# Optimization experiments

Hardware: AMD Instinct MI355X
Metric: run time of the kernel (lower is better)

## Reference

```python
import jax, jax.numpy as jnp
import numpy as np

B, IDF, CDF, SIZE, H, L = 32, 64, 256, 32, 8, 256
SS = SIZE * SIZE  # size*size = 1024


def setup_inputs() -> dict:
    key = jax.random.key(0)
    k1, k2, k3 = jax.random.split(key, 3)
    return {
        "weightedContext": jax.random.normal(k1, (B, IDF, SS), dtype=jnp.float32),
        "context": jax.random.normal(k2, (B, CDF, L), dtype=jnp.float32),
        # per-head conv1x1 weights: [H, size*size, cdf]
        "W": jax.random.normal(k3, (H, SS, CDF), dtype=jnp.float32) * 0.02,
        "ih": SIZE,
        "iw": SIZE,
    }


def reference(weightedContext, context, W, ih, iw):
    batch, idf = weightedContext.shape[0], weightedContext.shape[1]
    # conv1x1 per head == per-head GEMM over channel dim: [B,H,SS,L]
    sourceC = jnp.einsum("hoc,bcl->bhol", W, context)
    # attention scores: [B,H,idf,L]
    attn = jnp.einsum("bio,bhol->bhil", weightedContext, sourceC)
    # softmax over sourceL (nn.Softmax() on 2D view -> dim=1 == L here)
    attn = jax.nn.softmax(attn, axis=-1)
    # weightedContext_T summed over heads: bmm(sourceC, attn^T) -> [B,idf,SS]
    ctx_out = jnp.einsum("bhol,bhil->bio", sourceC, attn)
    ctx_out = ctx_out.reshape(batch, idf, ih, iw)
    # attnOut: per-head attn transposed [B,L,idf], summed over heads
    attn_out = jnp.sum(attn, axis=1).transpose(0, 2, 1)
    return ctx_out, attn_out
```

## Files before the change

kernel.cpp:

```cpp
#include <hip/hip_runtime.h>
#include <hip/hip_bf16.h>

#define BB 32
#define IDF 64
#define CDF 256
#define SSZ 1024
#define NH 8
#define LL 256
#define KHC 2048

typedef __attribute__((ext_vector_type(8))) _Float16 half8v;
typedef __attribute__((ext_vector_type(4))) float f32x4;

#define GLDS16(g, l) __builtin_amdgcn_global_load_lds(                        \
    (const __attribute__((address_space(1))) void*)(g),                       \
    (__attribute__((address_space(3))) void*)(l), 16, 0, 0)

#define WAIT_ENTER3(NFULL, NHALF)                                             \
  { if (ks < NSTEP - 2)                                                       \
      asm volatile("s_waitcnt vmcnt(" #NFULL ")" ::: "memory");               \
    else if (ks == NSTEP - 2)                                                 \
      asm volatile("s_waitcnt vmcnt(" #NHALF ")" ::: "memory");               \
    else                                                                      \
      asm volatile("s_waitcnt vmcnt(0)" ::: "memory");                        \
    __builtin_amdgcn_s_barrier();                                             \
    __builtin_amdgcn_sched_barrier(0); }
#define BAR_EXIT()                                                            \
  { __builtin_amdgcn_sched_barrier(0);                                        \
    __builtin_amdgcn_s_barrier();                                             \
    __builtin_amdgcn_sched_barrier(0); }
#define LDS_BAR()                                                             \
  { asm volatile("s_waitcnt lgkmcnt(0)" ::: "memory");                        \
    __builtin_amdgcn_s_barrier();                                             \
    __builtin_amdgcn_sched_barrier(0); }

__device__ inline unsigned short f2h(float x) {
  _Float16 h = (_Float16)x;
  return *reinterpret_cast<unsigned short*>(&h);
}
__device__ inline float h2f(unsigned short u) {
  _Float16 h = *reinterpret_cast<_Float16*>(&u);
  return (float)h;
}

__global__ __launch_bounds__(256) void k_prep(const float* __restrict__ wc,
                                              const float* __restrict__ W,
                                              const float* __restrict__ ctx,
                                              unsigned short* __restrict__ wc16,
                                              unsigned short* __restrict__ W16,
                                              unsigned short* __restrict__ ctx16,
                                              unsigned short* __restrict__ Wt16,
                                              unsigned short* __restrict__ cT16) {
  __shared__ float Tt[64][65];
  int blk0 = blockIdx.x;
  int t = threadIdx.x;
  if (blk0 < 6144) {
    int sel = blk0 >> 11;
    int idx = ((blk0 & 2047) * 256 + t) * 4;
    const float* src = (sel == 0) ? wc : (sel == 1) ? W : ctx;
    unsigned short* d = (sel == 0) ? wc16 : (sel == 1) ? W16 : ctx16;
    float4 v = *reinterpret_cast<const float4*>(&src[idx]);
    __align__(8) unsigned short h[4] = {f2h(v.x), f2h(v.y), f2h(v.z), f2h(v.w)};
    *reinterpret_cast<int2*>(&d[idx]) = *reinterpret_cast<int2*>(h);
  } else if (blk0 < 6656) {
    int blk = blk0 - 6144;
    int h = blk >> 6, ot = (blk >> 2) & 15, cq = blk & 3;
    int og = ot * 64, cg = cq * 64;
    int o_l = t >> 4, c4 = (t & 15) * 4;
#pragma unroll
    for (int p = 0; p < 4; ++p) {
      int o = o_l + 16 * p;
      float4 v = *reinterpret_cast<const float4*>(
          &W[((size_t)h * SSZ + og + o) * CDF + cg + c4]);
      Tt[c4 + 0][o] = v.x; Tt[c4 + 1][o] = v.y;
      Tt[c4 + 2][o] = v.z; Tt[c4 + 3][o] = v.w;
    }
    __syncthreads();
    int c_l = t >> 2;
#pragma unroll
    for (int p = 0; p < 4; ++p) {
      int o0 = ((t & 3) + 4 * p) * 4;
      __align__(8) unsigned short hv[4];
#pragma unroll
      for (int j = 0; j < 4; ++j) hv[j] = f2h(Tt[c_l][o0 + j]);
      size_t base = ((size_t)h * CDF + cg + c_l) * SSZ + og + o0;
      *reinterpret_cast<int2*>(&Wt16[base]) = *reinterpret_cast<int2*>(hv);
    }
  } else {
    int blk = blk0 - 6656;
    int b = blk >> 4, cq = (blk >> 2) & 3, lt = blk & 3;
    int cg = cq * 64, lg = lt * 64;
    int c_l = t >> 4, l4 = (t & 15) * 4;
#pragma unroll
    for (int p = 0; p < 4; ++p) {
      int c = c_l + 16 * p;
      float4 v = *reinterpret_cast<const float4*>(
          &ctx[((size_t)b * CDF + cg + c) * LL + lg + l4]);
      Tt[l4 + 0][c] = v.x; Tt[l4 + 1][c] = v.y;
      Tt[l4 + 2][c] = v.z; Tt[l4 + 3][c] = v.w;
    }
    __syncthreads();
    int l_l = t >> 2;
#pragma unroll
    for (int p = 0; p < 4; ++p) {
      int c0 = ((t & 3) + 4 * p) * 4;
      __align__(8) unsigned short hv[4];
#pragma unroll
      for (int j = 0; j < 4; ++j) hv[j] = f2h(Tt[l_l][c0 + j]);
      size_t base = ((size_t)b * LL + lg + l_l) * CDF + cg + c0;
      *reinterpret_cast<int2*>(&cT16[base]) = *reinterpret_cast<int2*>(hv);
    }
  }
}

__device__ __forceinline__ void st_p1(short* dst, const short* gA, const short* gB,
                                      int wave, int lane, int k0) {
#pragma unroll
  for (int j = 0; j < 3; ++j) {
    int inst = wave * 3 + j;
    const short* src; int toff, rb;
    if (inst < 4)       { src = gA; toff = 0;     rb = inst * 16; }
    else if (inst < 20) { src = gB; toff = 2048;  rb = (inst - 4) * 16; }
    else                { src = gA; toff = 10240; rb = (inst - 20) * 16; }
    int r  = rb + (lane >> 2);
    int gc = (lane & 3) ^ ((r >> 1) & 3);
    GLDS16(src + (size_t)r * SSZ + k0 + gc * 8, dst + toff + rb * 32);
  }
}
__device__ __forceinline__ void st_pB(short* dst, const short* gB, int ld,
                                      int wave, int lane, int k0) {
#pragma unroll
  for (int j = 0; j < 2; ++j) {
    int inst = wave * 2 + j;
    int rb = inst * 16;
    int r  = rb + (lane >> 2);
    int gc = (lane & 3) ^ ((r >> 1) & 3);
    GLDS16(gB + (size_t)r * ld + k0 + gc * 8, dst + 2048 + rb * 32);
  }
}

__global__ __launch_bounds__(512) void k123(const unsigned short* __restrict__ wc16,
                                            const unsigned short* __restrict__ Wt16,
                                            const unsigned short* __restrict__ cT16,
                                            const unsigned short* __restrict__ ctx16,
                                            unsigned short* __restrict__ P16,
                                            unsigned short* __restrict__ N216) {
  __shared__ __align__(16) short S[3 * 12288 + 16384];
  short* M_lds = &S[3 * 12288];

  int bh = blockIdx.x;
  int b = bh >> 3, h = bh & 7;
  int t = threadIdx.x;
  int lane = t & 63, wave = t >> 6;
  int ln15 = lane & 15, kh = lane >> 4;
  int rowq = (lane >> 4) * 4;

  const short* gA = (const short*)wc16 + (size_t)b * IDF * SSZ;
  const short* gB = (const short*)Wt16 + (size_t)h * CDF * SSZ;
  const short* gT = (const short*)cT16 + (size_t)b * LL * CDF;
  const short* gC = (const short*)ctx16 + (size_t)b * CDF * LL;

  int offA[4], offB[2], rowM[4], rmask[4];
#pragma unroll
  for (int r = 0; r < 4; ++r) {
    int row = r * 16 + ln15;
    offA[r] = row * 32 + ((kh ^ ((row >> 1) & 3)) * 8);
    rowM[r] = row * 256;
    rmask[r] = row & 7;
  }
#pragma unroll
  for (int c = 0; c < 2; ++c) {
    int row = wave * 32 + c * 16 + ln15;
    offB[c] = 2048 + row * 32 + ((kh ^ ((row >> 1) & 3)) * 8);
  }

  f32x4 acc[4][2] = {};

  st_p1(&S[0],         gA, gB, wave, lane, 0);
  st_p1(&S[12288],     gA, gB, wave, lane, 32);
  st_p1(&S[2 * 12288], gA, gB, wave, lane, 64);
  int cur = 0;
  {
    const int NSTEP = 32;
#pragma unroll 1
    for (int ks = 0; ks < NSTEP; ++ks) {
      short* Sc = &S[cur * 12288];
      WAIT_ENTER3(6, 3)
      half8v fa[4], fb[2];
#pragma unroll
      for (int r = 0; r < 4; ++r)
        fa[r] = *reinterpret_cast<const half8v*>(&Sc[offA[r]]);
#pragma unroll
      for (int c = 0; c < 2; ++c)
        fb[c] = *reinterpret_cast<const half8v*>(&Sc[offB[c]]);
      __builtin_amdgcn_s_setprio(1);
#pragma unroll
      for (int r = 0; r < 4; ++r)
#pragma unroll
        for (int c = 0; c < 2; ++c)
          acc[r][c] = __builtin_amdgcn_mfma_f32_16x16x32_f16(fa[r], fb[c], acc[r][c], 0, 0, 0);
      __builtin_amdgcn_s_setprio(0);
      BAR_EXIT()
      if (ks + 3 < NSTEP)
        st_p1(Sc, gA, gB, wave, lane, (ks + 3) * 32);
      cur = (cur == 2) ? 0 : cur + 1;
    }
  }
#pragma unroll
  for (int r = 0; r < 4; ++r)
#pragma unroll
    for (int c = 0; c < 2; ++c)
#pragma unroll
      for (int reg = 0; reg < 4; ++reg) {
        int row = r * 16 + rowq + reg;
        int col = wave * 32 + c * 16 + ln15;
        M_lds[row * 256 + ((((col >> 3) ^ (row & 7)) << 3) + (col & 7))] =
            (short)f2h(acc[r][c][reg]);
      }
  LDS_BAR()

#pragma unroll
  for (int r = 0; r < 4; ++r)
#pragma unroll
    for (int c = 0; c < 2; ++c) acc[r][c] = (f32x4){0.f, 0.f, 0.f, 0.f};
  st_pB(&S[0],         gT, CDF, wave, lane, 0);
  st_pB(&S[12288],     gT, CDF, wave, lane, 32);
  st_pB(&S[2 * 12288], gT, CDF, wave, lane, 64);
  cur = 0;
  {
    const int NSTEP = 8;
#pragma unroll 1
    for (int ks = 0; ks < NSTEP; ++ks) {
      short* Sc = &S[cur * 12288];
      WAIT_ENTER3(4, 2)
      half8v fa[4], fb[2];
#pragma unroll
      for (int r = 0; r < 4; ++r) {
        int ck = ((ks * 4 + kh) ^ rmask[r]) << 3;
        fa[r] = *reinterpret_cast<const half8v*>(&M_lds[rowM[r] + ck]);
      }
#pragma unroll
      for (int c = 0; c < 2; ++c)
        fb[c] = *reinterpret_cast<const half8v*>(&Sc[offB[c]]);
      __builtin_amdgcn_s_setprio(1);
#pragma unroll
      for (int r = 0; r < 4; ++r)
#pragma unroll
        for (int c = 0; c < 2; ++c)
          acc[r][c] = __builtin_amdgcn_mfma_f32_16x16x32_f16(fa[r], fb[c], acc[r][c], 0, 0, 0);
      __builtin_amdgcn_s_setprio(0);
      BAR_EXIT()
      if (ks + 3 < NSTEP)
        st_pB(Sc, gT, CDF, wave, lane, (ks + 3) * 32);
      cur = (cur == 2) ? 0 : cur + 1;
    }
  }

  st_pB(&S[0],         gC, LL, wave, lane, 0);
  st_pB(&S[12288],     gC, LL, wave, lane, 32);
  st_pB(&S[2 * 12288], gC, LL, wave, lane, 64);

  float* pm = reinterpret_cast<float*>(M_lds);
  float gmax[4][4], ginv[4][4];
#pragma unroll
  for (int r = 0; r < 4; ++r)
#pragma unroll
    for (int reg = 0; reg < 4; ++reg) {
      float m = fmaxf(acc[r][0][reg], acc[r][1][reg]);
#pragma unroll
      for (int msk = 8; msk >= 1; msk >>= 1) m = fmaxf(m, __shfl_xor(m, msk, 64));
      if (ln15 == 0) pm[(r * 16 + rowq + reg) * 8 + wave] = m;
    }
  LDS_BAR()
#pragma unroll
  for (int r = 0; r < 4; ++r)
#pragma unroll
    for (int reg = 0; reg < 4; ++reg) {
      int row = r * 16 + rowq + reg;
      float4 p0 = *reinterpret_cast<const float4*>(&pm[row * 8]);
      float4 p1 = *reinterpret_cast<const float4*>(&pm[row * 8 + 4]);
      gmax[r][reg] = fmaxf(fmaxf(fmaxf(p0.x, p0.y), fmaxf(p0.z, p0.w)),
                           fmaxf(fmaxf(p1.x, p1.y), fmaxf(p1.z, p1.w)));
    }
  LDS_BAR()
#pragma unroll
  for (int r = 0; r < 4; ++r)
#pragma unroll
    for (int reg = 0; reg < 4; ++reg) {
      acc[r][0][reg] = __expf(acc[r][0][reg] - gmax[r][reg]);
      acc[r][1][reg] = __expf(acc[r][1][reg] - gmax[r][reg]);
      float s = acc[r][0][reg] + acc[r][1][reg];
#pragma unroll
      for (int msk = 8; msk >= 1; msk >>= 1) s += __shfl_xor(s, msk, 64);
      if (ln15 == 0) pm[(r * 16 + rowq + reg) * 8 + wave] = s;
    }
  LDS_BAR()
#pragma unroll
  for (int r = 0; r < 4; ++r)
#pragma unroll
    for (int reg = 0; reg < 4; ++reg) {
      int row = r * 16 + rowq + reg;
      float4 p0 = *reinterpret_cast<const float4*>(&pm[row * 8]);
      float4 p1 = *reinterpret_cast<const float4*>(&pm[row * 8 + 4]);
      ginv[r][reg] = 1.f / (p0.x + p0.y + p0.z + p0.w + p1.x + p1.y + p1.z + p1.w);
    }
  LDS_BAR()

  size_t pbase = (size_t)bh * IDF * LL;
#pragma unroll
  for (int r = 0; r < 4; ++r)
#pragma unroll
    for (int c = 0; c < 2; ++c)
#pragma unroll
      for (int reg = 0; reg < 4; ++reg) {
        float p = acc[r][c][reg] * ginv[r][reg];
        int row = r * 16 + rowq + reg;
        int col = wave * 32 + c * 16 + ln15;
        unsigned short ph = f2h(p);
        P16[pbase + (size_t)row * LL + col] = ph;
        M_lds[row * 256 + ((((col >> 3) ^ (row & 7)) << 3) + (col & 7))] = (short)ph;
      }
  LDS_BAR()

#pragma unroll
  for (int r = 0; r < 4; ++r)
#pragma unroll
    for (int c = 0; c < 2; ++c) acc[r][c] = (f32x4){0.f, 0.f, 0.f, 0.f};
  cur = 0;
  {
    const int NSTEP = 8;
#pragma unroll 1
    for (int ks = 0; ks < NSTEP; ++ks) {
      short* Sc = &S[cur * 12288];
      WAIT_ENTER3(4, 2)
      half8v fa[4], fb[2];
#pragma unroll
      for (int r = 0; r < 4; ++r) {
        int ck = ((ks * 4 + kh) ^ rmask[r]) << 3;
        fa[r] = *reinterpret_cast<const half8v*>(&M_lds[rowM[r] + ck]);
      }
#pragma unroll
      for (int c = 0; c < 2; ++c)
        fb[c] = *reinterpret_cast<const half8v*>(&Sc[offB[c]]);
      __builtin_amdgcn_s_setprio(1);
#pragma unroll
      for (int r = 0; r < 4; ++r)
#pragma unroll
        for (int c = 0; c < 2; ++c)
          acc[r][c] = __builtin_amdgcn_mfma_f32_16x16x32_f16(fa[r], fb[c], acc[r][c], 0, 0, 0);
      __builtin_amdgcn_s_setprio(0);
      BAR_EXIT()
      if (ks + 3 < NSTEP)
        st_pB(Sc, gC, LL, wave, lane, (ks + 3) * 32);
      cur = (cur == 2) ? 0 : cur + 1;
    }
  }

  size_t nbase = (size_t)b * IDF * KHC + h * CDF;
#pragma unroll
  for (int r = 0; r < 4; ++r)
#pragma unroll
    for (int c = 0; c < 2; ++c)
#pragma unroll
      for (int reg = 0; reg < 4; ++reg) {
        size_t idx = nbase + (size_t)(r * 16 + rowq + reg) * KHC + wave * 32 + c * 16 + ln15;
        N216[idx] = f2h(acc[r][c][reg]);
      }
}

__device__ __forceinline__ void k4_stage(short* dst,
                                         const short* gA, const short* gB,
                                         int wave, int lane, int kk0, int obase) {
  int h4 = kk0 >> 8, cb = kk0 & 255;
#pragma unroll
  for (int j = 0; j < 3; ++j) {
    int inst = wave * 3 + j;
    if (inst < 4) {
      int rb = inst * 16;
      int r  = rb + (lane >> 2);
      int gc = (lane & 3) ^ ((r >> 1) & 3);
      GLDS16(gA + (size_t)r * KHC + kk0 + gc * 8, dst + rb * 32);
    } else {
      int rb = (inst - 4) * 16;
      int r  = rb + (lane >> 2);
      int gc = (lane & 3) ^ ((r >> 1) & 3);
      GLDS16(gB + (size_t)(h4 * SSZ + obase + r) * CDF + cb + gc * 8,
             dst + 2048 + rb * 32);
    }
  }
}

__global__ __launch_bounds__(256) void k4_mfma(const unsigned short* __restrict__ N216,
                                               const unsigned short* __restrict__ W16,
                                               float* __restrict__ out0,
                                               float* __restrict__ out1) {
  __shared__ __align__(16) short S[3 * 6144];

  int blk = blockIdx.x;
  int g = blk >> 8;
  int r8 = blk & 255;
  int b = r8 >> 3, ot = r8 & 7;
  int obase = ot * 128;
  int t = threadIdx.x;
  int lane = t & 63, wave = t >> 6;
  int ln15 = lane & 15, kh = lane >> 4;

  const short* gA = (const short*)N216 + (size_t)b * IDF * KHC;
  const short* gB = (const short*)W16;

  int offA[4], offB[2];
#pragma unroll
  for (int r = 0; r < 4; ++r) {
    int row = r * 16 + ln15;
    offA[r] = row * 32 + ((kh ^ ((row >> 1) & 3)) * 8);
  }
#pragma unroll
  for (int c = 0; c < 2; ++c) {
    int row = wave * 32 + c * 16 + ln15;
    offB[c] = 2048 + row * 32 + ((kh ^ ((row >> 1) & 3)) * 8);
  }

  int kbase = g * (KHC / 2);
  f32x4 acc[4][2] = {};

  k4_stage(&S[0],        gA, gB, wave, lane, kbase, obase);
  k4_stage(&S[6144],     gA, gB, wave, lane, kbase + 32, obase);
  k4_stage(&S[2 * 6144], gA, gB, wave, lane, kbase + 64, obase);
  int cur = 0;

  const int NSTEP = 32;
#pragma unroll 1
  for (int ks = 0; ks < NSTEP; ++ks) {
    short* Sc = &S[cur * 6144];
    WAIT_ENTER3(6, 3)
    half8v fa[4], fb[2];
#pragma unroll
    for (int r = 0; r < 4; ++r)
      fa[r] = *reinterpret_cast<const half8v*>(&Sc[offA[r]]);
#pragma unroll
    for (int c = 0; c < 2; ++c)
      fb[c] = *reinterpret_cast<const half8v*>(&Sc[offB[c]]);
    __builtin_amdgcn_s_setprio(1);
#pragma unroll
    for (int r = 0; r < 4; ++r)
#pragma unroll
      for (int c = 0; c < 2; ++c)
        acc[r][c] = __builtin_amdgcn_mfma_f32_16x16x32_f16(fa[r], fb[c], acc[r][c], 0, 0, 0);
    __builtin_amdgcn_s_setprio(0);
    BAR_EXIT()
    if (ks + 3 < NSTEP)
      k4_stage(Sc, gA, gB, wave, lane, kbase + (ks + 3) * 32, obase);
    cur = (cur == 2) ? 0 : cur + 1;
  }

  float* dst = (g == 0) ? out0 : out1;
  int rowq = (lane >> 4) * 4;
#pragma unroll
  for (int r = 0; r < 4; ++r)
#pragma unroll
    for (int c = 0; c < 2; ++c)
#pragma unroll
      for (int reg = 0; reg < 4; ++reg)
        dst[((size_t)b * IDF + r * 16 + rowq + reg) * SSZ +
            obase + wave * 32 + c * 16 + ln15] = acc[r][c][reg];
}

__global__ __launch_bounds__(256) void k_epi(const unsigned short* __restrict__ P16,
                                             float* __restrict__ outa,
                                             float* __restrict__ out,
                                             const float* __restrict__ Pbuf) {
  int blk0 = blockIdx.x;
  int tid = threadIdx.x;
  if (blk0 >= 128) {
    int idx = (blk0 - 128) * 256 + tid;
    float4 a = reinterpret_cast<float4*>(out)[idx];
    float4 p = reinterpret_cast<const float4*>(Pbuf)[idx];
    a.x += p.x; a.y += p.y; a.z += p.z; a.w += p.w;
    reinterpret_cast<float4*>(out)[idx] = a;
    return;
  }
  __shared__ float T[64][65];
  int b = blk0 >> 2, lt = blk0 & 3;
  int l0 = lt * 64;
  float4 acc[4];
#pragma unroll
  for (int p = 0; p < 4; ++p) acc[p] = make_float4(0.f, 0.f, 0.f, 0.f);
  for (int h = 0; h < NH; ++h) {
    size_t src = (size_t)(b * NH + h) * IDF * LL;
#pragma unroll
    for (int p = 0; p < 4; ++p) {
      int f = tid + p * 256;
      int i = f >> 4, lc = (f & 15) * 4;
      ushort4 u = *reinterpret_cast<const ushort4*>(&P16[src + i * LL + l0 + lc]);
      acc[p].x += h2f(u.x); acc[p].y += h2f(u.y);
      acc[p].z += h2f(u.z); acc[p].w += h2f(u.w);
    }
  }
#pragma unroll
  for (int p = 0; p < 4; ++p) {
    int f = tid + p * 256;
    int i = f >> 4, lc = (f & 15) * 4;
    T[i][lc + 0] = acc[p].x; T[i][lc + 1] = acc[p].y;
    T[i][lc + 2] = acc[p].z; T[i][lc + 3] = acc[p].w;
  }
  __syncthreads();
#pragma unroll
  for (int p = 0; p < 4; ++p) {
    int f = tid + p * 256;
    int lr = f >> 4, ic = (f & 15) * 4;
    float4 v = {T[ic + 0][lr], T[ic + 1][lr], T[ic + 2][lr], T[ic + 3][lr]};
    *reinterpret_cast<float4*>(&outa[((size_t)b * LL + l0 + lr) * IDF + ic]) = v;
  }
}

extern "C" void kernel_launch(void* const* d_in, const int* in_sizes, int n_in,
                              void* d_out, int out_size, void* d_ws, size_t ws_size,
                              hipStream_t stream) {
  const float* wc  = (const float*)d_in[0];
  const float* ctx = (const float*)d_in[1];
  const float* W   = (const float*)d_in[2];
  float* out = (float*)d_out;

  const size_t NE = 2097152;
  const size_t NM = 4194304;
  unsigned short* p = (unsigned short*)d_ws;
  unsigned short *wc16 = p;   p += NE;
  unsigned short *Wt16 = p;   p += NE;
  unsigned short *W16  = p;   p += NE;
  unsigned short *ctx16 = p;  p += NE;
  unsigned short *cT16 = p;   p += NE;
  unsigned short *P16  = p;   p += NM;
  unsigned short *N216 = p;   p += NM;
  float* Pbuf = (float*)p;

  k_prep  <<<7168, 256, 0, stream>>>(wc, W, ctx, wc16, W16, ctx16, Wt16, cT16);
  k123    <<<BB * NH, 512, 0, stream>>>(wc16, Wt16, cT16, ctx16, P16, N216);
  k4_mfma <<<512, 256, 0, stream>>>(N216, W16, out, Pbuf);
  k_epi   <<<2176, 256, 0, stream>>>(P16, out + (size_t)BB * IDF * SSZ, out, Pbuf);
}
```

Measured before the change: 79.78 us.

## Split first GEMM into separate kernel with doubled grid for more parallelism

The first GEMM stage (wc × W per head, K=1024) moves out of the fused k123 kernel into a new k1_mfma kernel. It launches 512 blocks of 256 threads, splitting the CDF dimension in half and writing an fp16 intermediate M16 to global memory. The remaining k23 kernel then streams M16 in place of the long K loop. The aim is better occupancy and CU utilisation than the 256 blocks that each ran a 32-step loop. The cost is an extra kernel launch and a global round trip for the 64x256 intermediate per (b,h).

```diff
diff --git a/kernel.cpp b/kernel.cpp
--- a/kernel.cpp
+++ b/kernel.cpp
@@ -113,18 +113,109 @@
   }
 }
 
-__device__ __forceinline__ void st_p1(short* dst, const short* gA, const short* gB,
+__device__ __forceinline__ void k1_stage(short* dst,
+                                         const short* gA, const short* gB,
+                                         int wave, int lane, int k0) {
+#pragma unroll
+  for (int j = 0; j < 3; ++j) {
+    int inst = wave * 3 + j;
+    if (inst < 4) {
+      int rb = inst * 16;
+      int r  = rb + (lane >> 2);
+      int gc = (lane & 3) ^ ((r >> 1) & 3);
+      GLDS16(gA + (size_t)r * SSZ + k0 + gc * 8, dst + rb * 32);
+    } else {
+      int rb = (inst - 4) * 16;
+      int r  = rb + (lane >> 2);
+      int gc = (lane & 3) ^ ((r >> 1) & 3);
+      GLDS16(gB + (size_t)r * SSZ + k0 + gc * 8, dst + 2048 + rb * 32);
+    }
+  }
+}
+
+__global__ __launch_bounds__(256) void k1_mfma(const unsigned short* __restrict__ wc16,
+                                               const unsigned short* __restrict__ Wt16,
+                                               unsigned short* __restrict__ M16) {
+  __shared__ __align__(16) short S[3 * 6144];
+
+  int blk = blockIdx.x;
+  int bh = blk >> 1, nh = blk & 1;
+  int b = bh >> 3, h = bh & 7;
+  int t = threadIdx.x;
+  int lane = t & 63, wave = t >> 6;
+  int ln15 = lane & 15, kh = lane >> 4;
+
+  const short* gA = (const short*)wc16 + (size_t)b * IDF * SSZ;
+  const short* gB = (const short*)Wt16 + (size_t)(h * CDF + nh * 128) * SSZ;
+
+  int offA[4], offB[2];
+#pragma unroll
+  for (int r = 0; r < 4; ++r) {
+    int row = r * 16 + ln15;
+    offA[r] = row * 32 + ((kh ^ ((row >> 1) & 3)) * 8);
+  }
+#pragma unroll
+  for (int c = 0; c < 2; ++c) {
+    int row = wave * 32 + c * 16 + ln15;
+    offB[c] = 2048 + row * 32 + ((kh ^ ((row >> 1) & 3)) * 8);
+  }
+
+  f32x4 acc[4][2] = {};
+  k1_stage(&S[0],        gA, gB, wave, lane, 0);
+  k1_stage(&S[6144],     gA, gB, wave, lane, 32);
+  k1_stage(&S[2 * 6144], gA, gB, wave, lane, 64);
+  int cur = 0;
+
+  const int NSTEP = 32;
+#pragma unroll 1
+  for (int ks = 0; ks < NSTEP; ++ks) {
+    short* Sc = &S[cur * 6144];
+    WAIT_ENTER3(6, 3)
+    half8v fa[4], fb[2];
+#pragma unroll
+    for (int r = 0; r < 4; ++r)
+      fa[r] = *reinterpret_cast<const half8v*>(&Sc[offA[r]]);
+#pragma unroll
+    for (int c = 0; c < 2; ++c)
+      fb[c] = *reinterpret_cast<const half8v*>(&Sc[offB[c]]);
+    __builtin_amdgcn_s_setprio(1);
+#pragma unroll
+    for (int r = 0; r < 4; ++r)
+#pragma unroll
+      for (int c = 0; c < 2; ++c)
+        acc[r][c] = __builtin_amdgcn_mfma_f32_16x16x32_f16(fa[r], fb[c], acc[r][c], 0, 0, 0);
+    __builtin_amdgcn_s_setprio(0);
+    BAR_EXIT()
+    if (ks + 3 < NSTEP)
+      k1_stage(Sc, gA, gB, wave, lane, (ks + 3) * 32);
+    cur = (cur == 2) ? 0 : cur + 1;
+  }
+
+  size_t obase = (size_t)bh * IDF * CDF + nh * 128;
+  int rowq = (lane >> 4) * 4;
+#pragma unroll
+  for (int r = 0; r < 4; ++r)
+#pragma unroll
+    for (int c = 0; c < 2; ++c)
+#pragma unroll
+      for (int reg = 0; reg < 4; ++reg) {
+        size_t idx = obase + (size_t)(r * 16 + rowq + reg) * CDF + wave * 32 + c * 16 + ln15;
+        M16[idx] = f2h(acc[r][c][reg]);
+      }
+}
+
+__device__ __forceinline__ void st_p2(short* dst, const short* gM, const short* gT,
                                       int wave, int lane, int k0) {
 #pragma unroll
   for (int j = 0; j < 3; ++j) {
     int inst = wave * 3 + j;
     const short* src; int toff, rb;
-    if (inst < 4)       { src = gA; toff = 0;     rb = inst * 16; }
-    else if (inst < 20) { src = gB; toff = 2048;  rb = (inst - 4) * 16; }
-    else                { src = gA; toff = 10240; rb = (inst - 20) * 16; }
+    if (inst < 4)       { src = gM; toff = 0;     rb = inst * 16; }
+    else if (inst < 20) { src = gT; toff = 2048;  rb = (inst - 4) * 16; }
+    else                { src = gM; toff = 10240; rb = (inst - 20) * 16; }
     int r  = rb + (lane >> 2);
     int gc = (lane & 3) ^ ((r >> 1) & 3);
-    GLDS16(src + (size_t)r * SSZ + k0 + gc * 8, dst + toff + rb * 32);
+    GLDS16(src + (size_t)r * CDF + k0 + gc * 8, dst + toff + rb * 32);
   }
 }
 __device__ __forceinline__ void st_pB(short* dst, const short* gB, int ld,
@@ -139,14 +230,13 @@
   }
 }
 
-__global__ __launch_bounds__(512) void k123(const unsigned short* __restrict__ wc16,
-                                            const unsigned short* __restrict__ Wt16,
-                                            const unsigned short* __restrict__ cT16,
-                                            const unsigned short* __restrict__ ctx16,
-                                            unsigned short* __restrict__ P16,
-                                            unsigned short* __restrict__ N216) {
+__global__ __launch_bounds__(512) void k23(const unsigned short* __restrict__ M16,
+                                           const unsigned short* __restrict__ cT16,
+                                           const unsigned short* __restrict__ ctx16,
+                                           unsigned short* __restrict__ P16,
+                                           unsigned short* __restrict__ N216) {
   __shared__ __align__(16) short S[3 * 12288 + 16384];
-  short* M_lds = &S[3 * 12288];
+  short* P_lds = &S[3 * 12288];
 
   int bh = blockIdx.x;
   int b = bh >> 3, h = bh & 7;
@@ -155,8 +245,7 @@
   int ln15 = lane & 15, kh = lane >> 4;
   int rowq = (lane >> 4) * 4;
 
-  const short* gA = (const short*)wc16 + (size_t)b * IDF * SSZ;
-  const short* gB = (const short*)Wt16 + (size_t)h * CDF * SSZ;
+  const short* gM = (const short*)M16 + (size_t)bh * IDF * CDF;
   const short* gT = (const short*)cT16 + (size_t)b * LL * CDF;
   const short* gC = (const short*)ctx16 + (size_t)b * CDF * LL;
 
@@ -176,12 +265,12 @@
 
   f32x4 acc[4][2] = {};
 
-  st_p1(&S[0],         gA, gB, wave, lane, 0);
-  st_p1(&S[12288],     gA, gB, wave, lane, 32);
-  st_p1(&S[2 * 12288], gA, gB, wave, lane, 64);
+  st_p2(&S[0],         gM, gT, wave, lane, 0);
+  st_p2(&S[12288],     gM, gT, wave, lane, 32);
+  st_p2(&S[2 * 12288], gM, gT, wave, lane, 64);
   int cur = 0;
   {
-    const int NSTEP = 32;
+    const int NSTEP = 8;
 #pragma unroll 1
     for (int ks = 0; ks < NSTEP; ++ks) {
       short* Sc = &S[cur * 12288];
@@ -202,56 +291,7 @@
       __builtin_amdgcn_s_setprio(0);
       BAR_EXIT()
       if (ks + 3 < NSTEP)
-        st_p1(Sc, gA, gB, wave, lane, (ks + 3) * 32);
-      cur = (cur == 2) ? 0 : cur + 1;
-    }
-  }
-#pragma unroll
-  for (int r = 0; r < 4; ++r)
-#pragma unroll
-    for (int c = 0; c < 2; ++c)
-#pragma unroll
-      for (int reg = 0; reg < 4; ++reg) {
-        int row = r * 16 + rowq + reg;
-        int col = wave * 32 + c * 16 + ln15;
-        M_lds[row * 256 + ((((col >> 3) ^ (row & 7)) << 3) + (col & 7))] =
-            (short)f2h(acc[r][c][reg]);
-      }
-  LDS_BAR()
-
-#pragma unroll
-  for (int r = 0; r < 4; ++r)
-#pragma unroll
-    for (int c = 0; c < 2; ++c) acc[r][c] = (f32x4){0.f, 0.f, 0.f, 0.f};
-  st_pB(&S[0],         gT, CDF, wave, lane, 0);
-  st_pB(&S[12288],     gT, CDF, wave, lane, 32);
-  st_pB(&S[2 * 12288], gT, CDF, wave, lane, 64);
-  cur = 0;
-  {
-    const int NSTEP = 8;
-#pragma unroll 1
-    for (int ks = 0; ks < NSTEP; ++ks) {
-      short* Sc = &S[cur * 12288];
-      WAIT_ENTER3(4, 2)
-      half8v fa[4], fb[2];
-#pragma unroll
-      for (int r = 0; r < 4; ++r) {
-        int ck = ((ks * 4 + kh) ^ rmask[r]) << 3;
-        fa[r] = *reinterpret_cast<const half8v*>(&M_lds[rowM[r] + ck]);
-      }
-#pragma unroll
-      for (int c = 0; c < 2; ++c)
-        fb[c] = *reinterpret_cast<const half8v*>(&Sc[offB[c]]);
-      __builtin_amdgcn_s_setprio(1);
-#pragma unroll
-      for (int r = 0; r < 4; ++r)
-#pragma unroll
-        for (int c = 0; c < 2; ++c)
-          acc[r][c] = __builtin_amdgcn_mfma_f32_16x16x32_f16(fa[r], fb[c], acc[r][c], 0, 0, 0);
-      __builtin_amdgcn_s_setprio(0);
-      BAR_EXIT()
-      if (ks + 3 < NSTEP)
-        st_pB(Sc, gT, CDF, wave, lane, (ks + 3) * 32);
+        st_p2(Sc, gM, gT, wave, lane, (ks + 3) * 32);
       cur = (cur == 2) ? 0 : cur + 1;
     }
   }
@@ -260,7 +300,7 @@
   st_pB(&S[12288],     gC, LL, wave, lane, 32);
   st_pB(&S[2 * 12288], gC, LL, wave, lane, 64);
 
-  float* pm = reinterpret_cast<float*>(M_lds);
+  float* pm = reinterpret_cast<float*>(P_lds);
   float gmax[4][4], ginv[4][4];
 #pragma unroll
   for (int r = 0; r < 4; ++r)
@@ -318,7 +358,7 @@
         int col = wave * 32 + c * 16 + ln15;
         unsigned short ph = f2h(p);
         P16[pbase + (size_t)row * LL + col] = ph;
-        M_lds[row * 256 + ((((col >> 3) ^ (row & 7)) << 3) + (col & 7))] = (short)ph;
+        P_lds[row * 256 + ((((col >> 3) ^ (row & 7)) << 3) + (col & 7))] = (short)ph;
       }
   LDS_BAR()
 
@@ -337,7 +377,7 @@
 #pragma unroll
       for (int r = 0; r < 4; ++r) {
         int ck = ((ks * 4 + kh) ^ rmask[r]) << 3;
-        fa[r] = *reinterpret_cast<const half8v*>(&M_lds[rowM[r] + ck]);
+        fa[r] = *reinterpret_cast<const half8v*>(&P_lds[rowM[r] + ck]);
       }
 #pragma unroll
       for (int c = 0; c < 2; ++c)
@@ -529,12 +569,14 @@
   unsigned short *W16  = p;   p += NE;
   unsigned short *ctx16 = p;  p += NE;
   unsigned short *cT16 = p;   p += NE;
+  unsigned short *M16  = p;   p += NM;
   unsigned short *P16  = p;   p += NM;
   unsigned short *N216 = p;   p += NM;
   float* Pbuf = (float*)p;
 
   k_prep  <<<7168, 256, 0, stream>>>(wc, W, ctx, wc16, W16, ctx16, Wt16, cT16);
-  k123    <<<BB * NH, 512, 0, stream>>>(wc16, Wt16, cT16, ctx16, P16, N216);
+  k1_mfma <<<BB * NH * 2, 256, 0, stream>>>(wc16, Wt16, M16);
+  k23     <<<BB * NH, 512, 0, stream>>>(M16, cT16, ctx16, P16, N216);
   k4_mfma <<<512, 256, 0, stream>>>(N216, W16, out, Pbuf);
   k_epi   <<<2176, 256, 0, stream>>>(P16, out + (size_t)BB * IDF * SSZ, out, Pbuf);
 }
```

New measurement: 82.25 us. 3.1% more time.

## Split k123 blocks over idf halves with 4 waves each to double grid size

Applied to the files above, without the earlier changes.

The fused attention kernel now launches two blocks per (batch, head), each handling 32 of the 64 idf rows with 256 threads (4 waves), and each wave covers 64 output columns instead of 32. Staging, LDS buffer sizes, wait counts and softmax reductions are resized to match. The aim is better CU occupancy: 512 blocks instead of 256 on a GPU with many CUs, plus less LDS per block. In exchange, the shared W/cT/ctx tiles (the B operand) are now loaded twice per (b,h), raising global and L2 traffic.

```diff
diff --git a/kernel.cpp b/kernel.cpp
--- a/kernel.cpp
+++ b/kernel.cpp
@@ -113,15 +113,17 @@
   }
 }
 
+#define BUF_SH 10240
+
 __device__ __forceinline__ void st_p1(short* dst, const short* gA, const short* gB,
                                       int wave, int lane, int k0) {
 #pragma unroll
-  for (int j = 0; j < 3; ++j) {
-    int inst = wave * 3 + j;
+  for (int j = 0; j < 5; ++j) {
+    int inst = wave * 5 + j;
     const short* src; int toff, rb;
-    if (inst < 4)       { src = gA; toff = 0;     rb = inst * 16; }
-    else if (inst < 20) { src = gB; toff = 2048;  rb = (inst - 4) * 16; }
-    else                { src = gA; toff = 10240; rb = (inst - 20) * 16; }
+    if (inst < 2)       { src = gA; toff = 0;    rb = inst * 16; }
+    else if (inst < 18) { src = gB; toff = 1024; rb = (inst - 2) * 16; }
+    else                { src = gA; toff = 9216; rb = (inst - 18) * 16; }
     int r  = rb + (lane >> 2);
     int gc = (lane & 3) ^ ((r >> 1) & 3);
     GLDS16(src + (size_t)r * SSZ + k0 + gc * 8, dst + toff + rb * 32);
@@ -130,74 +132,75 @@
 __device__ __forceinline__ void st_pB(short* dst, const short* gB, int ld,
                                       int wave, int lane, int k0) {
 #pragma unroll
-  for (int j = 0; j < 2; ++j) {
-    int inst = wave * 2 + j;
-    int rb = inst * 16;
+  for (int j = 0; j < 4; ++j) {
+    int rb = (wave * 4 + j) * 16;
     int r  = rb + (lane >> 2);
     int gc = (lane & 3) ^ ((r >> 1) & 3);
-    GLDS16(gB + (size_t)r * ld + k0 + gc * 8, dst + 2048 + rb * 32);
-  }
-}
-
-__global__ __launch_bounds__(512) void k123(const unsigned short* __restrict__ wc16,
+    GLDS16(gB + (size_t)r * ld + k0 + gc * 8, dst + 1024 + rb * 32);
+  }
+}
+
+__global__ __launch_bounds__(256) void k123(const unsigned short* __restrict__ wc16,
                                             const unsigned short* __restrict__ Wt16,
                                             const unsigned short* __restrict__ cT16,
                                             const unsigned short* __restrict__ ctx16,
                                             unsigned short* __restrict__ P16,
                                             unsigned short* __restrict__ N216) {
-  __shared__ __align__(16) short S[3 * 12288 + 16384];
-  short* M_lds = &S[3 * 12288];
-
-  int bh = blockIdx.x;
+  __shared__ __align__(16) short S[3 * BUF_SH + 8192];
+  short* P_lds = &S[3 * BUF_SH];
+
+  int blk = blockIdx.x;
+  int bh = blk >> 1, ih = blk & 1;
   int b = bh >> 3, h = bh & 7;
+  int ibase = ih * 32;
   int t = threadIdx.x;
   int lane = t & 63, wave = t >> 6;
   int ln15 = lane & 15, kh = lane >> 4;
   int rowq = (lane >> 4) * 4;
 
-  const short* gA = (const short*)wc16 + (size_t)b * IDF * SSZ;
+  const short* gA = (const short*)wc16 + (size_t)(b * IDF + ibase) * SSZ;
   const short* gB = (const short*)Wt16 + (size_t)h * CDF * SSZ;
   const short* gT = (const short*)cT16 + (size_t)b * LL * CDF;
   const short* gC = (const short*)ctx16 + (size_t)b * CDF * LL;
 
-  int offA[4], offB[2], rowM[4], rmask[4];
-#pragma unroll
-  for (int r = 0; r < 4; ++r) {
+  int offA[2], offB[4], rowM[2], rmask[2];
+#pragma unroll
+  for (int r = 0; r < 2; ++r) {
     int row = r * 16 + ln15;
     offA[r] = row * 32 + ((kh ^ ((row >> 1) & 3)) * 8);
     rowM[r] = row * 256;
     rmask[r] = row & 7;
   }
 #pragma unroll
-  for (int c = 0; c < 2; ++c) {
-    int row = wave * 32 + c * 16 + ln15;
-    offB[c] = 2048 + row * 32 + ((kh ^ ((row >> 1) & 3)) * 8);
-  }
-
-  f32x4 acc[4][2] = {};
-
-  st_p1(&S[0],         gA, gB, wave, lane, 0);
-  st_p1(&S[12288],     gA, gB, wave, lane, 32);
-  st_p1(&S[2 * 12288], gA, gB, wave, lane, 64);
+  for (int c = 0; c < 4; ++c) {
+    int row = wave * 64 + c * 16 + ln15;
+    offB[c] = 1024 + row * 32 + ((kh ^ ((row >> 1) & 3)) * 8);
+  }
+
+  f32x4 acc[2][4] = {};
+
+  st_p1(&S[0],           gA, gB, wave, lane, 0);
+  st_p1(&S[BUF_SH],      gA, gB, wave, lane, 32);
+  st_p1(&S[2 * BUF_SH],  gA, gB, wave, lane, 64);
   int cur = 0;
   {
     const int NSTEP = 32;
 #pragma unroll 1
     for (int ks = 0; ks < NSTEP; ++ks) {
-      short* Sc = &S[cur * 12288];
-      WAIT_ENTER3(6, 3)
-      half8v fa[4], fb[2];
-#pragma unroll
-      for (int r = 0; r < 4; ++r)
+      short* Sc = &S[cur * BUF_SH];
+      WAIT_ENTER3(10, 5)
+      half8v fa[2], fb[4];
+#pragma unroll
+      for (int r = 0; r < 2; ++r)
         fa[r] = *reinterpret_cast<const half8v*>(&Sc[offA[r]]);
 #pragma unroll
-      for (int c = 0; c < 2; ++c)
+      for (int c = 0; c < 4; ++c)
         fb[c] = *reinterpret_cast<const half8v*>(&Sc[offB[c]]);
       __builtin_amdgcn_s_setprio(1);
 #pragma unroll
-      for (int r = 0; r < 4; ++r)
-#pragma unroll
-        for (int c = 0; c < 2; ++c)
+      for (int r = 0; r < 2; ++r)
+#pragma unroll
+        for (int c = 0; c < 4; ++c)
           acc[r][c] = __builtin_amdgcn_mfma_f32_16x16x32_f16(fa[r], fb[c], acc[r][c], 0, 0, 0);
       __builtin_amdgcn_s_setprio(0);
       BAR_EXIT()
@@ -207,46 +210,46 @@
     }
   }
 #pragma unroll
-  for (int r = 0; r < 4; ++r)
-#pragma unroll
-    for (int c = 0; c < 2; ++c)
+  for (int r = 0; r < 2; ++r)
+#pragma unroll
+    for (int c = 0; c < 4; ++c)
 #pragma unroll
       for (int reg = 0; reg < 4; ++reg) {
         int row = r * 16 + rowq + reg;
-        int col = wave * 32 + c * 16 + ln15;
-        M_lds[row * 256 + ((((col >> 3) ^ (row & 7)) << 3) + (col & 7))] =
+        int col = wave * 64 + c * 16 + ln15;
+        P_lds[row * 256 + ((((col >> 3) ^ (row & 7)) << 3) + (col & 7))] =
             (short)f2h(acc[r][c][reg]);
       }
   LDS_BAR()
 
 #pragma unroll
-  for (int r = 0; r < 4; ++r)
-#pragma unroll
-    for (int c = 0; c < 2; ++c) acc[r][c] = (f32x4){0.f, 0.f, 0.f, 0.f};
-  st_pB(&S[0],         gT, CDF, wave, lane, 0);
-  st_pB(&S[12288],     gT, CDF, wave, lane, 32);
-  st_pB(&S[2 * 12288], gT, CDF, wave, lane, 64);
+  for (int r = 0; r < 2; ++r)
+#pragma unroll
+    for (int c = 0; c < 4; ++c) acc[r][c] = (f32x4){0.f, 0.f, 0.f, 0.f};
+  st_pB(&S[0],          gT, CDF, wave, lane, 0);
+  st_pB(&S[BUF_SH],     gT, CDF, wave, lane, 32);
+  st_pB(&S[2 * BUF_SH], gT, CDF, wave, lane, 64);
   cur = 0;
   {
     const int NSTEP = 8;
 #pragma unroll 1
     for (int ks = 0; ks < NSTEP; ++ks) {
-      short* Sc = &S[cur * 12288];
-      WAIT_ENTER3(4, 2)
-      half8v fa[4], fb[2];
-#pragma unroll
-      for (int r = 0; r < 4; ++r) {
+      short* Sc = &S[cur * BUF_SH];
+      WAIT_ENTER3(8, 4)
+      half8v fa[2], fb[4];
+#pragma unroll
+      for (int r = 0; r < 2; ++r) {
         int ck = ((ks * 4 + kh) ^ rmask[r]) << 3;
-        fa[r] = *reinterpret_cast<const half8v*>(&M_lds[rowM[r] + ck]);
+        fa[r] = *reinterpret_cast<const half8v*>(&P_lds[rowM[r] + ck]);
       }
 #pragma unroll
-      for (int c = 0; c < 2; ++c)
+      for (int c = 0; c < 4; ++c)
         fb[c] = *reinterpret_cast<const half8v*>(&Sc[offB[c]]);
       __builtin_amdgcn_s_setprio(1);
 #pragma unroll
-      for (int r = 0; r < 4; ++r)
-#pragma unroll
-        for (int c = 0; c < 2; ++c)
+      for (int r = 0; r < 2; ++r)
+#pragma unroll
+        for (int c = 0; c < 4; ++c)
           acc[r][c] = __builtin_amdgcn_mfma_f32_16x16x32_f16(fa[r], fb[c], acc[r][c], 0, 0, 0);
       __builtin_amdgcn_s_setprio(0);
       BAR_EXIT()
@@ -256,97 +259,98 @@
     }
   }
 
-  st_pB(&S[0],         gC, LL, wave, lane, 0);
-  st_pB(&S[12288],     gC, LL, wave, lane, 32);
-  st_pB(&S[2 * 12288], gC, LL, wave, lane, 64);
-
-  float* pm = reinterpret_cast<float*>(M_lds);
-  float gmax[4][4], ginv[4][4];
-#pragma unroll
-  for (int r = 0; r < 4; ++r)
+  st_pB(&S[0],          gC, LL, wave, lane, 0);
+  st_pB(&S[BUF_SH],     gC, LL, wave, lane, 32);
+  st_pB(&S[2 * BUF_SH], gC, LL, wave, lane, 64);
+
+  float* pm = reinterpret_cast<float*>(P_lds);
+  float gmax[2][4], ginv[2][4];
+#pragma unroll
+  for (int r = 0; r < 2; ++r)
 #pragma unroll
     for (int reg = 0; reg < 4; ++reg) {
-      float m = fmaxf(acc[r][0][reg], acc[r][1][reg]);
+      float m = fmaxf(fmaxf(acc[r][0][reg], acc[r][1][reg]),
+                      fmaxf(acc[r][2][reg], acc[r][3][reg]));
 #pragma unroll
       for (int msk = 8; msk >= 1; msk >>= 1) m = fmaxf(m, __shfl_xor(m, msk, 64));
-      if (ln15 == 0) pm[(r * 16 + rowq + reg) * 8 + wave] = m;
+      if (ln15 == 0) pm[(r * 16 + rowq + reg) * 4 + wave] = m;
     }
   LDS_BAR()
 #pragma unroll
-  for (int r = 0; r < 4; ++r)
+  for (int r = 0; r < 2; ++r)
 #pragma unroll
     for (int reg = 0; reg < 4; ++reg) {
       int row = r * 16 + rowq + reg;
-      float4 p0 = *reinterpret_cast<const float4*>(&pm[row * 8]);
-      float4 p1 = *reinterpret_cast<const float4*>(&pm[row * 8 + 4]);
-      gmax[r][reg] = fmaxf(fmaxf(fmaxf(p0.x, p0.y), fmaxf(p0.z, p0.w)),
-                           fmaxf(fmaxf(p1.x, p1.y), fmaxf(p1.z, p1.w)));
+      float4 p0 = *reinterpret_cast<const float4*>(&pm[row * 4]);
+      gmax[r][reg] = fmaxf(fmaxf(p0.x, p0.y), fmaxf(p0.z, p0.w));
     }
   LDS_BAR()
 #pragma unroll
-  for (int r = 0; r < 4; ++r)
+  for (int r = 0; r < 2; ++r)
 #pragma unroll
     for (int reg = 0; reg < 4; ++reg) {
-      acc[r][0][reg] = __expf(acc[r][0][reg] - gmax[r][reg]);
-      acc[r][1][reg] = __expf(acc[r][1][reg] - gmax[r][reg]);
-      float s = acc[r][0][reg] + acc[r][1][reg];
+      float s = 0.f;
+#pragma unroll
+      for (int c = 0; c < 4; ++c) {
+        acc[r][c][reg] = __expf(acc[r][c][reg] - gmax[r][reg]);
+        s += acc[r][c][reg];
+      }
 #pragma unroll
       for (int msk = 8; msk >= 1; msk >>= 1) s += __shfl_xor(s, msk, 64);
-      if (ln15 == 0) pm[(r * 16 + rowq + reg) * 8 + wave] = s;
+      if (ln15 == 0) pm[(r * 16 + rowq + reg) * 4 + wave] = s;
     }
   LDS_BAR()
 #pragma unroll
-  for (int r = 0; r < 4; ++r)
+  for (int r = 0; r < 2; ++r)
 #pragma unroll
     for (int reg = 0; reg < 4; ++reg) {
       int row = r * 16 + rowq + reg;
-      float4 p0 = *reinterpret_cast<const float4*>(&pm[row * 8]);
-      float4 p1 = *reinterpret_cast<const float4*>(&pm[row * 8 + 4]);
-      ginv[r][reg] = 1.f / (p0.x + p0.y + p0.z + p0.w + p1.x + p1.y + p1.z + p1.w);
+      float4 p0 = *reinterpret_cast<const float4*>(&pm[row * 4]);
+      ginv[r][reg] = 1.f / (p0.x + p0.y + p0.z + p0.w);
     }
   LDS_BAR()
 
-  size_t pbase = (size_t)bh * IDF * LL;
-#pragma unroll
-  for (int r = 0; r < 4; ++r)
-#pragma unroll
-    for (int c = 0; c < 2; ++c)
+  size_t pbase = (size_t)bh * IDF * LL + (size_t)ibase * LL;
+#pragma unroll
+  for (int r = 0; r < 2; ++r)
+#pragma unroll
+    for (int c = 0; c < 4; ++c)
 #pragma unroll
       for (int reg = 0; reg < 4; ++reg) {
         float p = acc[r][c][reg] * ginv[r][reg];
         int row = r * 16 + rowq + reg;
-        int col = wave * 32 + c * 16 + ln15;
+        int col = wave * 64 + c * 16 + ln15;
         unsigned short ph = f2h(p);
         P16[pbase + (size_t)row * LL + col] = ph;
-        M_lds[row * 256 + ((((col >> 3) ^ (row & 7)) << 3) + (col & 7))] = (short)ph;
+        P_lds[row * 256 + ((((col >> 3) ^ (row & 7)) << 3) + (col & 7))] = (short)ph;
       }
   LDS_BAR()
 
 #pragma unroll
-  for (int r = 0; r < 4; ++r)
-#pragma unroll
-    for (int c = 0; c < 2; ++c) acc[r][c] = (f32x4){0.f, 0.f, 0.f, 0.f};
+  for (int r = 0; r < 2; ++r)
+#pragma unroll
+    for (int c = 0; c < 4; ++c) acc[r][c] = (f32x4){0.f, 0.f, 0.f, 0.f};
   cur = 0;
   {
     const int NSTEP = 8;
 #pragma unroll 1
     for (int ks = 0; ks < NSTEP; ++ks) {
-      short* Sc = &S[cur * 12288];
-      WAIT_ENTER3(4, 2)
-      half8v fa[4], fb[2];
-#pragma unroll
-      for (int r = 0; r < 4; ++r) {
+      short* Sc = &S[cur * BUF_SH];
+      WAIT_ENTER3(8, 4)
+      half8v fa[2], fb[4];
+#pragma unroll
+      for (int r = 0; r < 2; ++r) {
         int ck = ((ks * 4 + kh) ^ rmask[r]) << 3;
-        fa[r] = *reinterpret_cast<const half8v*>(&M_lds[rowM[r] + ck]);
+        fa[r] = *reinterpret_cast<const half8v*>(&P_lds[rowM[r] + ck]);
       }
 #pragma unroll
-      for (int c = 0; c < 2; ++c)
+      for (int c = 0; c < 4; ++c)
         fb[c] = *reinterpret_cast<const half8v*>(&Sc[offB[c]]);
       __builtin_amdgcn_s_setprio(1);
 #pragma unroll
-      for (int r = 0; r < 4; ++r)
-#pragma unroll
-        for (int c = 0; c < 2; ++c)
+      for (int r = 0; r < 2; ++r)
+#pragma unroll
+        for (int c = 0; c < 4; ++c)
           acc[r][c] = __builtin_amdgcn_mfma_f32_16x16x32_f16(fa[r], fb[c], acc[r][c], 0, 0, 0);
       __builtin_amdgcn_s_setprio(0);
       BAR_EXIT()
@@ -356,15 +360,16 @@
     }
   }
 
-  size_t nbase = (size_t)b * IDF * KHC + h * CDF;
-#pragma unroll
-  for (int r = 0; r < 4; ++r)
-#pragma unroll
-    for (int c = 0; c < 2; ++c)
+  size_t nbase = (size_t)b * IDF * KHC + (size_t)ibase * KHC + h * CDF;
+#pragma unroll
+  for (int r = 0; r < 2; ++r)
+#pragma unroll
+    for (int c = 0; c < 4; ++c)
 #pragma unroll
       for (int reg = 0; reg < 4; ++reg) {
-        size_t idx = nbase + (size_t)(r * 16 + rowq + reg) * KHC + wave * 32 + c * 16 + ln15;
-        N216[idx] = f2h(acc[r][c][reg]);
+        int row = r * 16 + rowq + reg;
+        int col = wave * 64 + c * 16 + ln15;
+        N216[nbase + (size_t)row * KHC + col] = f2h(acc[r][c][reg]);
       }
 }
 
@@ -534,7 +539,7 @@
   float* Pbuf = (float*)p;
 
   k_prep  <<<7168, 256, 0, stream>>>(wc, W, ctx, wc16, W16, ctx16, Wt16, cT16);
-  k123    <<<BB * NH, 512, 0, stream>>>(wc16, Wt16, cT16, ctx16, P16, N216);
+  k123    <<<BB * NH * 2, 256, 0, stream>>>(wc16, Wt16, cT16, ctx16, P16, N216);
   k4_mfma <<<512, 256, 0, stream>>>(N216, W16, out, Pbuf);
   k_epi   <<<2176, 256, 0, stream>>>(P16, out + (size_t)BB * IDF * SSZ, out, Pbuf);
 }
```

New measurement: 80.28 us. No clear change (+0.6%).
